# Performance work log

Hardware: AMD Instinct MI355X
Metric: run time of the kernel (lower is better)

The kernel has to match this reference:

```python
import jax, jax.numpy as jnp
import numpy as np

D_MODEL = 1024
N_HEAD = 16
D_HEAD = 64
M_FEAT = 128  # d_kernel_map


def _gen_projection_matrix(m, d, rng):
    # Performer-style: stacked orthogonal blocks scaled by chi-distributed row norms
    blocks = []
    for _ in range(m // d):
        q, _ = np.linalg.qr(rng.standard_normal((d, d)))
        blocks.append(q.T)
    rem = m % d
    if rem > 0:
        q, _ = np.linalg.qr(rng.standard_normal((d, d)))
        blocks.append(q.T[:rem])
    mat = np.vstack(blocks)
    multiplier = np.linalg.norm(rng.standard_normal((m, d)), axis=1, keepdims=True)
    return (mat * multiplier).astype(np.float32)


def setup_inputs() -> dict:
    key = jax.random.key(0)
    ks = jax.random.split(key, 6)
    B, L = 4, 4096
    rng = np.random.default_rng(0)
    hd = N_HEAD * D_HEAD
    x = jax.random.normal(ks[0], (B, L, D_MODEL), dtype=jnp.float32)
    pos_ft = jax.random.normal(ks[1], (B, L, D_MODEL), dtype=jnp.float32)
    pos_ft_slopes = jax.random.normal(ks[2], (B, L, D_MODEL), dtype=jnp.float32)
    W_v = jax.random.normal(ks[3], (D_MODEL, hd), dtype=jnp.float32) / np.sqrt(D_MODEL)
    W_o = jax.random.normal(ks[4], (hd, D_MODEL), dtype=jnp.float32) / np.sqrt(hd)
    pos_ft_weight = jax.random.normal(ks[5], (D_MODEL, hd), dtype=jnp.float32)
    pos_ft_scale = jnp.ones((1, 1, N_HEAD, 1), dtype=jnp.float32)
    head_range = 1.0 / N_HEAD
    offs = (np.arange(0, 1.0, head_range) + head_range / 2.0).astype(np.float32)
    pos_ft_offsets = jnp.asarray(offs).reshape(1, 1, N_HEAD, 1)
    proj = jnp.asarray(_gen_projection_matrix(M_FEAT, D_HEAD, rng))
    return {"x": x, "pos_ft": pos_ft, "pos_ft_slopes": pos_ft_slopes,
            "W_v": W_v, "W_o": W_o, "pos_ft_weight": pos_ft_weight,
            "pos_ft_scale": pos_ft_scale, "pos_ft_offsets": pos_ft_offsets,
            "proj": proj}


def _fourier_kernel(data, proj):
    # data: [B,L,H,D]; proj: [M,D] -> features [B,L,H,2M]
    data_normalizer = 1.0 / data.shape[-1] ** 0.25
    ratio = 1.0 / proj.shape[0] ** 0.5
    data_dash = jnp.einsum('blhd,md->blhm', data_normalizer * data, proj)
    return jnp.concatenate([ratio * jnp.sin(data_dash), ratio * jnp.cos(data_dash)], axis=-1)


def reference(x, pos_ft, pos_ft_slopes, W_v, W_o, pos_ft_weight, pos_ft_scale, pos_ft_offsets, proj):
    B, L, _ = x.shape
    v = (x @ W_v).reshape(B, L, N_HEAD, D_HEAD)
    pos_proj = (pos_ft @ pos_ft_weight).reshape(B, L, N_HEAD, D_HEAD)
    slope_proj = (pos_ft_slopes @ pos_ft_weight).reshape(B, L, N_HEAD, D_HEAD)
    query_pos = pos_ft_scale * pos_proj
    key_pos = query_pos + pos_ft_offsets * (pos_ft_scale * slope_proj)
    q_prime = _fourier_kernel(query_pos, proj)   # [B,L,H,2M]
    k_prime = _fourier_kernel(key_pos, proj)
    kv = jnp.einsum('blhm,blhd->bhmd', k_prime, v)
    z = jnp.einsum('blhm,bhmd->blhd', q_prime, kv)
    norm_factor = jnp.linalg.norm(slope_proj, axis=-1, keepdims=True) / float(L)
    z = (z * norm_factor).reshape(B, L, N_HEAD * D_HEAD)
    # dropout is identity in eval mode
    return z @ W_o
```

## Files before the change

### kernel.cpp

```cpp
#include <hip/hip_runtime.h>
#include <hip/hip_bf16.h>
#include <stdint.h>


typedef _Float16 hx8 __attribute__((ext_vector_type(8)));
typedef _Float16 hx4 __attribute__((ext_vector_type(4)));
typedef float    fx4 __attribute__((ext_vector_type(4)));

#define H_   16
#define D_   64
#define L_   4096
#define B_   4
#define KV_SPLIT 16

__device__ __forceinline__ void g2l16(const _Float16* g, _Float16* l) {
  __builtin_amdgcn_global_load_lds(
      (const __attribute__((address_space(1))) void*)g,
      (__attribute__((address_space(3))) void*)l, 16, 0, 0);
}

__global__ __launch_bounds__(256) void wt2_k(const float* __restrict__ W0,
                                             _Float16* __restrict__ T0,
                                             const float* __restrict__ W1,
                                             _Float16* __restrict__ T1) {
  const float* W = blockIdx.z ? W1 : W0;
  _Float16* WT   = blockIdx.z ? T1 : T0;
  __shared__ float tile[64][65];
  int t = threadIdx.x; int c = t & 63; int r0 = t >> 6;
  int bx = blockIdx.x * 64, by = blockIdx.y * 64;
  for (int r = r0; r < 64; r += 4) tile[r][c] = W[(long)(by + r) * 1024 + bx + c];
  __syncthreads();
  for (int r = r0; r < 64; r += 4)
    WT[(long)(bx + r) * 1024 + by + c] = (_Float16)tile[c][r];
}

__global__ __launch_bounds__(256) void wpf3_k(const float* __restrict__ W,
                                              _Float16* __restrict__ WT3) {
  __shared__ float tile[64][65];
  int t = threadIdx.x; int c = t & 63; int r0 = t >> 6;
  int bx = blockIdx.x * 64, by = blockIdx.y * 64;
  for (int r = r0; r < 64; r += 4) tile[r][c] = W[(long)(by + r) * 1024 + bx + c];
  __syncthreads();
  for (int r = r0; r < 64; r += 4) {
    float x = tile[c][r];
    _Float16 hi = (_Float16)x;
    _Float16 lo = (_Float16)(x - (float)hi);
    long base = (long)(bx + r) * 3072 + by + c;
    WT3[base] = hi; WT3[base + 1024] = hi; WT3[base + 2048] = lo;
  }
}

__global__ __launch_bounds__(256) void proj6_k(const float* __restrict__ proj,
                                               _Float16* __restrict__ proj6T) {
  int i = blockIdx.x * 256 + threadIdx.x;
  if (i >= 8192) return;
  int m = i >> 6, d = i & 63;
  float p = 0.35355339059327373f * proj[i];
  _Float16 hi = (_Float16)p;
  _Float16 lo = (_Float16)(p - (float)hi);
  long b = (long)m * 384 + d;
  proj6T[b]       = hi; proj6T[b + 64]  = hi; proj6T[b + 128] = lo;
  proj6T[b + 192] = hi; proj6T[b + 256] = hi; proj6T[b + 320] = lo;
}

__global__ __launch_bounds__(256) void zero_k(float* __restrict__ p, int n4) {
  int i = blockIdx.x * 256 + threadIdx.x;
  int stride = gridDim.x * 256;
  fx4 z = {0.f, 0.f, 0.f, 0.f};
  for (; i < n4; i += stride) ((fx4*)p)[i] = z;
}

__global__ __launch_bounds__(256) void cvt_hilo2_k(const float* __restrict__ pos,
                                                   const float* __restrict__ slp,
                                                   _Float16* __restrict__ ph2,
                                                   _Float16* __restrict__ sh2) {
  const float* in = blockIdx.y ? slp : pos;
  _Float16* out   = blockIdx.y ? sh2 : ph2;
  long i = (long)blockIdx.x * 256 + threadIdx.x;
  long idx = i * 8;
  int row = (int)(idx >> 10), c = (int)(idx & 1023);
  fx4 a = *(const fx4*)&in[idx];
  fx4 b = *(const fx4*)&in[idx + 4];
  hx8 hi, lo;
#pragma unroll
  for (int e = 0; e < 4; ++e) {
    _Float16 h0 = (_Float16)a[e]; hi[e] = h0;     lo[e]     = (_Float16)(a[e] - (float)h0);
    _Float16 h1 = (_Float16)b[e]; hi[4 + e] = h1; lo[4 + e] = (_Float16)(b[e] - (float)h1);
  }
  *(hx8*)&out[(long)row * 2048 + c]        = hi;
  *(hx8*)&out[(long)row * 2048 + 1024 + c] = lo;
}

__global__ __launch_bounds__(256) void cvt16_k(const float* __restrict__ in,
                                               _Float16* __restrict__ out, long n8) {
  long i = (long)blockIdx.x * 256 + threadIdx.x;
  if (i >= n8) return;
  long idx = i * 8;
  fx4 a = *(const fx4*)&in[idx];
  fx4 b = *(const fx4*)&in[idx + 4];
  hx8 h;
#pragma unroll
  for (int e = 0; e < 4; ++e) { h[e] = (_Float16)a[e]; h[4 + e] = (_Float16)b[e]; }
  *(hx8*)&out[idx] = h;
}

template<int BM, int BN, int AMODE, int SECSH, int EPI, int BMODE, typename OUT_T>
__global__ __launch_bounds__(256) void gemm_bt_k(
    const void* __restrict__ Av, const _Float16* __restrict__ BT,
    OUT_T* __restrict__ C, int K, int lda, int ldb, int ldc,
    long sAb, long sAh, long sBb, long sBh, long sCb, long sCh,
    const float* __restrict__ norms, const float* __restrict__ scp,
    const float* __restrict__ ofp, const float* __restrict__ Pprev,
    float* __restrict__ nout)
{
  __shared__ __align__(16) _Float16 sA[BM * 64];
  __shared__ __align__(16) _Float16 sB[BN * 64];
  const int t = threadIdx.x;
  const int lane = t & 63;
  const int w = t >> 6;
  const int wm = w >> 1, wn = w & 1;
  const int by = blockIdx.x, bx = blockIdx.y, bz = blockIdx.z;
  long aoff64 = (long)(bz >> 4) * sAb + (long)(bz & 15) * sAh;
  if constexpr (AMODE == 5) aoff64 = 0;
  const _Float16* BT16 = BT;
  const float*    B32  = (const float*)BT;
  if constexpr (BMODE == 0) BT16 += (long)(bz >> 4) * sBb + (long)(bz & 15) * sBh;
  else                      B32  += (long)(bz >> 4) * sBb + (long)(bz & 15) * sBh;
  C += (long)(bz >> 4) * sCb + (long)(bz & 15) * sCh;
  const _Float16* A16 = (const _Float16*)Av + aoff64;
  if constexpr (EPI == 4) {
    if (bz & 15) A16 = (const _Float16*)Pprev + aoff64;
  }
  constexpr int WTM = BM / 32, WTN = BN / 32;
  fx4 acc[WTM][WTN];
#pragma unroll
  for (int i = 0; i < WTM; ++i)
#pragma unroll
    for (int j = 0; j < WTN; ++j) acc[i][j] = (fx4){0.f, 0.f, 0.f, 0.f};

  const int trow = t >> 3;
  const int kc8  = ((t & 7) ^ (trow & 7)) * 8;
  int aoff[BM / 32];
#pragma unroll
  for (int i = 0; i < BM / 32; ++i)
    aoff[i] = (by * BM + i * 32 + trow) * lda + kc8;
  int boff[BN / 32];
#pragma unroll
  for (int i = 0; i < BN / 32; ++i)
    boff[i] = (bx * BN + i * 32 + trow) * ldb + kc8;
  _Float16* sAdst[BM / 32];
  _Float16* sBdst[BN / 32];
#pragma unroll
  for (int i = 0; i < BM / 32; ++i) sAdst[i] = &sA[(i * 256 + (w << 6)) * 8];
#pragma unroll
  for (int i = 0; i < BN / 32; ++i) sBdst[i] = &sB[(i * 256 + (w << 6)) * 8];

  int Klim = K;
  if constexpr (AMODE == 5) { if ((bz & 1) == 0) Klim >>= 1; }

  for (int k0 = 0; k0 < Klim; k0 += 64) {
    __syncthreads();
    {
      int cb;
      if constexpr (AMODE == 4) {
        int sec = k0 >> SECSH;
        cb = (k0 & ((1 << SECSH) - 1)) + (sec == 1 ? (1 << SECSH) : 0);
      } else if constexpr (AMODE == 5) {
        int sec = k0 >> SECSH;
        cb = ((sec == 1 || sec == 4) ? 64 : 0) + (sec >= 3 ? (int)sAb : 0);
      } else cb = k0;
#pragma unroll
      for (int i = 0; i < BM / 32; ++i) g2l16(A16 + (aoff[i] + cb), sAdst[i]);
    }
    if constexpr (BMODE == 0) {
#pragma unroll
      for (int i = 0; i < BN / 32; ++i) g2l16(BT16 + (boff[i] + k0), sBdst[i]);
    } else {
#pragma unroll
      for (int i = 0; i < BN / 32; ++i) {
        const float* src = B32 + (boff[i] + k0);
        fx4 v0 = *(const fx4*)src;
        fx4 v1 = *(const fx4*)(src + 4);
        hx8 hv;
#pragma unroll
        for (int e = 0; e < 4; ++e) { hv[e] = (_Float16)v0[e]; hv[4 + e] = (_Float16)v1[e]; }
        *(hx8*)&sB[(i * 256 + t) * 8] = hv;
      }
    }
    __syncthreads();
#pragma unroll
    for (int kk = 0; kk < 64; kk += 32) {
      hx8 af[WTM], bf[WTN];
      int kcb = (kk >> 3) + (lane >> 4);
#pragma unroll
      for (int i = 0; i < WTM; ++i) {
        int r = wm * (BM / 2) + i * 16 + (lane & 15);
        af[i] = *(const hx8*)&sA[(r * 8 + (kcb ^ (r & 7))) * 8];
      }
#pragma unroll
      for (int j = 0; j < WTN; ++j) {
        int r = wn * (BN / 2) + j * 16 + (lane & 15);
        bf[j] = *(const hx8*)&sB[(r * 8 + (kcb ^ (r & 7))) * 8];
      }
#pragma unroll
      for (int i = 0; i < WTM; ++i)
#pragma unroll
        for (int j = 0; j < WTN; ++j)
          acc[i][j] = __builtin_amdgcn_mfma_f32_16x16x32_f16(af[i], bf[j], acc[i][j], 0, 0, 0);
    }
  }
  if constexpr (EPI == 0) {
#pragma unroll
    for (int i = 0; i < WTM; ++i) {
#pragma unroll
      for (int j = 0; j < WTN; ++j) {
        int rowb = by * BM + wm * (BM / 2) + i * 16 + ((lane >> 4) << 2);
        int col  = bx * BN + wn * (BN / 2) + j * 16 + (lane & 15);
#pragma unroll
        for (int r = 0; r < 4; ++r)
          C[(long)(rowb + r) * ldc + col] = (OUT_T)acc[i][j][r];
      }
    }
  } else if constexpr (EPI == 1) {
    const float inv2pi = 0.15915494309189535f;
    const float ratio  = 0.08838834764831845f;
    const bool useN = ((bz & 15) == 0);
#pragma unroll
    for (int i = 0; i < WTM; ++i) {
#pragma unroll
      for (int j = 0; j < WTN; ++j) {
        int rowb = by * BM + wm * (BM / 2) + i * 16 + ((lane >> 4) << 2);
        int col  = bx * BN + wn * (BN / 2) + j * 16 + (lane & 15);
#pragma unroll
        for (int r = 0; r < 4; ++r) {
          int row = rowb + r;
          float rn = ratio * (useN ? norms[row] : 1.0f);
          long ob = ((long)(row & 15) * 4096 + (row >> 4)) * 256;
          float v = acc[i][j][r] * inv2pi;
          v -= floorf(v);
          C[ob + col]       = (OUT_T)(rn * __builtin_amdgcn_sinf(v));
          C[ob + 128 + col] = (OUT_T)(rn * __builtin_amdgcn_cosf(v));
        }
      }
    }
  } else {
    const int h = ((bx * BN) >> 6) + wn;
    const float sc = scp[h];
    _Float16* C16 = (_Float16*)C;
    if ((bz & 15) == 0) {
#pragma unroll
      for (int i = 0; i < WTM; ++i) {
#pragma unroll
        for (int j = 0; j < WTN; ++j) {
          int rowb = by * BM + wm * (BM / 2) + i * 16 + ((lane >> 4) << 2);
          int d    = j * 16 + (lane & 15);
#pragma unroll
          for (int r = 0; r < 4; ++r) {
            float v = sc * acc[i][j][r];
            long a = ((long)(rowb + r) * 16 + h) * 128 + d;
            _Float16 hi = (_Float16)v;
            C16[a]      = hi;
            C16[a + 64] = (_Float16)(v - (float)hi);
          }
        }
      }
    } else {
      const float osc = ofp[h] * sc;
#pragma unroll
      for (int i = 0; i < WTM; ++i) {
        float sq[4] = {0.f, 0.f, 0.f, 0.f};
        int rowb = by * BM + wm * (BM / 2) + i * 16 + ((lane >> 4) << 2);
#pragma unroll
        for (int j = 0; j < WTN; ++j) {
          int d = j * 16 + (lane & 15);
#pragma unroll
          for (int r = 0; r < 4; ++r) {
            float a0 = acc[i][j][r];
            sq[r] += a0 * a0;
            float v = osc * a0;
            long a = ((long)(rowb + r) * 16 + h) * 128 + d;
            _Float16 hi = (_Float16)v;
            C16[a]      = hi;
            C16[a + 64] = (_Float16)(v - (float)hi);
          }
        }
#pragma unroll
        for (int r = 0; r < 4; ++r) {
          float s = sq[r];
          s += __shfl_xor(s, 1); s += __shfl_xor(s, 2);
          s += __shfl_xor(s, 4); s += __shfl_xor(s, 8);
          if ((lane & 15) == 0)
            nout[(long)(rowb + r) * 16 + h] = sqrtf(s) * (1.0f / 4096.0f);
        }
      }
    }
  }
}

__global__ __launch_bounds__(256) void kv_k(const _Float16* __restrict__ Kp,
                                            const _Float16* __restrict__ Vhb,
                                            float* __restrict__ kvacc)
{
  __shared__ __align__(16) _Float16 sK[256 * 72];
  __shared__ __align__(16) _Float16 sV[64 * 72];
  const int t = threadIdx.x, lane = t & 63, w = t >> 6;
  const int h = blockIdx.x;
  const int l0 = blockIdx.y * (L_ / KV_SPLIT);
  fx4 acc[4][4];
#pragma unroll
  for (int i = 0; i < 4; ++i)
#pragma unroll
    for (int j = 0; j < 4; ++j) acc[i][j] = (fx4){0.f, 0.f, 0.f, 0.f};
  const _Float16* Kbase = Kp + (long)h * L_ * 256;
  for (int kt = 0; kt < L_ / KV_SPLIT; kt += 64) {
    __syncthreads();
#pragma unroll
    for (int it = 0; it < 2; ++it) {
      int idx = t + it * 256;
      int m8 = idx & 31, bl = (idx >> 5) << 2;
      const _Float16* src = &Kbase[(long)(l0 + kt + bl) * 256 + m8 * 8];
      hx8 r0 = *(const hx8*)(src);
      hx8 r1 = *(const hx8*)(src + 256);
      hx8 r2 = *(const hx8*)(src + 512);
      hx8 r3 = *(const hx8*)(src + 768);
      int kx = (m8 & 7) << 4;
#pragma unroll
      for (int e = 0; e < 8; ++e) {
        hx4 v; v[0] = r0[e]; v[1] = r1[e]; v[2] = r2[e]; v[3] = r3[e];
        int byte = (((m8 * 8 + e) * 72 + bl) * 2) ^ kx;
        *(hx4*)((char*)sK + byte) = v;
      }
    }
    if (t < 128) {
      int d8 = t & 7, bl = (t >> 3) << 2;
      const _Float16* src = &Vhb[(long)(l0 + kt + bl) * 1024 + h * 64 + d8 * 8];
      hx8 r0 = *(const hx8*)(src);
      hx8 r1 = *(const hx8*)(src + 1024);
      hx8 r2 = *(const hx8*)(src + 2048);
      hx8 r3 = *(const hx8*)(src + 3072);
      int kx = d8 << 4;
#pragma unroll
      for (int e = 0; e < 8; ++e) {
        hx4 v; v[0] = r0[e]; v[1] = r1[e]; v[2] = r2[e]; v[3] = r3[e];
        int byte = (((d8 * 8 + e) * 72 + bl) * 2) ^ kx;
        *(hx4*)((char*)sV + byte) = v;
      }
    }
    __syncthreads();
#pragma unroll
    for (int kk = 0; kk < 64; kk += 32) {
      hx8 af[4], bf[4];
      int lfr = kk + ((lane >> 4) << 3);
#pragma unroll
      for (int i = 0; i < 4; ++i) {
        int r = i * 16 + (lane & 15);
        af[i] = *(const hx8*)((const char*)sV +
                ((((r * 72 + lfr) * 2)) ^ (((r >> 3) & 7) << 4)));
      }
#pragma unroll
      for (int j = 0; j < 4; ++j) {
        int r = w * 64 + j * 16 + (lane & 15);
        bf[j] = *(const hx8*)((const char*)sK +
                ((((r * 72 + lfr) * 2)) ^ (((r >> 3) & 7) << 4)));
      }
#pragma unroll
      for (int i = 0; i < 4; ++i)
#pragma unroll
        for (int j = 0; j < 4; ++j)
          acc[i][j] = __builtin_amdgcn_mfma_f32_16x16x32_f16(af[i], bf[j], acc[i][j], 0, 0, 0);
    }
  }
  float* obase = kvacc + (long)h * (64 * 256);
#pragma unroll
  for (int i = 0; i < 4; ++i)
#pragma unroll
    for (int j = 0; j < 4; ++j) {
      int d0 = i * 16 + ((lane >> 4) << 2);
      int m  = w * 64 + j * 16 + (lane & 15);
#pragma unroll
      for (int r = 0; r < 4; ++r)
        atomicAdd(&obase[(long)(d0 + r) * 256 + m], acc[i][j][r]);
    }
}

extern "C" void kernel_launch(void* const* d_in, const int* in_sizes, int n_in,
                              void* d_out, int out_size, void* d_ws, size_t ws_size,
                              hipStream_t stream) {
  const float* x     = (const float*)d_in[0];
  const float* pos   = (const float*)d_in[1];
  const float* slp   = (const float*)d_in[2];
  const float* Wv    = (const float*)d_in[3];
  const float* Wo    = (const float*)d_in[4];
  const float* Wpf   = (const float*)d_in[5];
  const float* scale = (const float*)d_in[6];
  const float* offs  = (const float*)d_in[7];
  const float* proj  = (const float*)d_in[8];
  float* out = (float*)d_out;
  char* ws = (char*)d_ws;

  size_t o = 0;
  auto alloc = [&](size_t bytes) { char* p = ws + o; o += (bytes + 255) & ~(size_t)255; return p; };
  _Float16* Pb2    = (_Float16*)alloc(33554432);
  _Float16* Sb2    = (_Float16*)alloc(33554432);
  _Float16* qpr    = (_Float16*)alloc(33554432);
  _Float16* kpr    = (_Float16*)alloc(33554432);
  _Float16* Vh     = (_Float16*)alloc(33554432);
  _Float16* Zb     = (_Float16*)alloc(33554432);
  _Float16* WvT    = (_Float16*)alloc(2097152);
  _Float16* WoT    = (_Float16*)alloc(2097152);
  _Float16* Wpf3T  = (_Float16*)alloc(6291456);
  _Float16* proj6T = (_Float16*)alloc(98304);
  float*    normsB = (float*)alloc(524288);
  float*    kvacc  = (float*)alloc(4194304);
  _Float16* ph2 = qpr;
  _Float16* sh2 = kpr;
  _Float16* xh  = Zb;
  (void)Sb2; (void)ws_size; (void)in_sizes; (void)n_in; (void)out_size;

  wt2_k<<<dim3(16, 16, 2), 256, 0, stream>>>(Wv, WvT, Wo, WoT);
  wpf3_k<<<dim3(16, 16), 256, 0, stream>>>(Wpf, Wpf3T);
  proj6_k<<<32, 256, 0, stream>>>(proj, proj6T);
  zero_k<<<256, 256, 0, stream>>>(kvacc, 1048576 / 4);
  cvt16_k<<<8192, 256, 0, stream>>>(x, xh, 2097152);

  gemm_bt_k<128, 128, 0, 0, 0, 0, _Float16><<<dim3(128, 8, 1), 256, 0, stream>>>(
      xh, WvT, Vh, 1024, 1024, 1024, 1024, 0, 0, 0, 0, 0, 0,
      nullptr, nullptr, nullptr, nullptr, nullptr);

  for (int sb = 0; sb < 2; ++sb) {
    const float* pos_sb = pos + (long)sb * 8192 * 1024;
    const float* slp_sb = slp + (long)sb * 8192 * 1024;
    cvt_hilo2_k<<<dim3(4096, 2), 256, 0, stream>>>(pos_sb, slp_sb, ph2, sh2);
    gemm_bt_k<128, 128, 4, 10, 4, 0, _Float16><<<dim3(64, 8, 2), 256, 0, stream>>>(
        ph2, Wpf3T, Pb2, 3072, 2048, 3072, 128, 0, 0, 0, 0, 0, 16777216L,
        nullptr, scale, offs, (const float*)sh2, normsB);

    for (int bb = 0; bb < 2; ++bb) {
      int b = sb * 2 + bb;
      _Float16* Vh_b  = Vh + (long)b * L_ * 1024;
      _Float16* Zb_b  = Zb + (long)b * L_ * 1024;
      float* kvacc_b  = kvacc + (long)b * H_ * 64 * 256;
      gemm_bt_k<128, 128, 5, 6, 1, 0, _Float16><<<dim3(512, 1, 2), 256, 0, stream>>>(
          Pb2 + (long)bb * 8388608, proj6T, qpr, 384, 128, 384, 0,
          16777216L , 0L, 0, 0, 0, 16777216L,
          normsB + (long)bb * 65536, nullptr, nullptr, nullptr, nullptr);
      kv_k<<<dim3(16, KV_SPLIT), 256, 0, stream>>>(kpr, Vh_b, kvacc_b);
      gemm_bt_k<128, 64, 0, 0, 0, 1, _Float16><<<dim3(32, 1, 16), 256, 0, stream>>>(
          qpr, (const _Float16*)kvacc_b, Zb_b, 256, 256, 256, 1024,
          0L, (long)L_ * 256, 0L, 16384L, 0L, 64L,
          nullptr, nullptr, nullptr, nullptr, nullptr);
    }
  }
  gemm_bt_k<128, 128, 0, 0, 0, 0, float><<<dim3(128, 8, 1), 256, 0, stream>>>(
      Zb, WoT, out, 1024, 1024, 1024, 1024, 0, 0, 0, 0, 0, 0,
      nullptr, nullptr, nullptr, nullptr, nullptr);
}
```

Before: 860.8 us.

## Fuse prep kernels and batch feature/kv/z stages across two batches per launch

Merges the five setup kernels (weight transposes, proj split, kv accumulator zeroing, x conversion) into one launch, with block ranges selecting the task. When the workspace is large enough, the Fourier feature GEMM, kv reduction and z GEMM each run once per pair of batches by widening the grid z dimension, which cuts launches and raises per-launch parallelism. It needs a bigger feature buffer and falls back to the per-batch loop otherwise.

```diff
diff --git a/kernel.cpp b/kernel.cpp
--- a/kernel.cpp
+++ b/kernel.cpp
@@ -19,55 +19,64 @@
       (__attribute__((address_space(3))) void*)l, 16, 0, 0);
 }
 
-__global__ __launch_bounds__(256) void wt2_k(const float* __restrict__ W0,
-                                             _Float16* __restrict__ T0,
-                                             const float* __restrict__ W1,
-                                             _Float16* __restrict__ T1) {
-  const float* W = blockIdx.z ? W1 : W0;
-  _Float16* WT   = blockIdx.z ? T1 : T0;
+__global__ __launch_bounds__(256) void prep_k(
+    const float* __restrict__ Wv, _Float16* __restrict__ WvT,
+    const float* __restrict__ Wo, _Float16* __restrict__ WoT,
+    const float* __restrict__ Wpf, _Float16* __restrict__ Wpf3T,
+    const float* __restrict__ proj, _Float16* __restrict__ proj6T,
+    float* __restrict__ kvacc, const float* __restrict__ x,
+    _Float16* __restrict__ xh)
+{
   __shared__ float tile[64][65];
-  int t = threadIdx.x; int c = t & 63; int r0 = t >> 6;
-  int bx = blockIdx.x * 64, by = blockIdx.y * 64;
-  for (int r = r0; r < 64; r += 4) tile[r][c] = W[(long)(by + r) * 1024 + bx + c];
-  __syncthreads();
-  for (int r = r0; r < 64; r += 4)
-    WT[(long)(bx + r) * 1024 + by + c] = (_Float16)tile[c][r];
-}
-
-__global__ __launch_bounds__(256) void wpf3_k(const float* __restrict__ W,
-                                              _Float16* __restrict__ WT3) {
-  __shared__ float tile[64][65];
-  int t = threadIdx.x; int c = t & 63; int r0 = t >> 6;
-  int bx = blockIdx.x * 64, by = blockIdx.y * 64;
-  for (int r = r0; r < 64; r += 4) tile[r][c] = W[(long)(by + r) * 1024 + bx + c];
-  __syncthreads();
-  for (int r = r0; r < 64; r += 4) {
-    float x = tile[c][r];
-    _Float16 hi = (_Float16)x;
-    _Float16 lo = (_Float16)(x - (float)hi);
-    long base = (long)(bx + r) * 3072 + by + c;
-    WT3[base] = hi; WT3[base + 1024] = hi; WT3[base + 2048] = lo;
-  }
-}
-
-__global__ __launch_bounds__(256) void proj6_k(const float* __restrict__ proj,
-                                               _Float16* __restrict__ proj6T) {
-  int i = blockIdx.x * 256 + threadIdx.x;
-  if (i >= 8192) return;
-  int m = i >> 6, d = i & 63;
-  float p = 0.35355339059327373f * proj[i];
-  _Float16 hi = (_Float16)p;
-  _Float16 lo = (_Float16)(p - (float)hi);
-  long b = (long)m * 384 + d;
-  proj6T[b]       = hi; proj6T[b + 64]  = hi; proj6T[b + 128] = lo;
-  proj6T[b + 192] = hi; proj6T[b + 256] = hi; proj6T[b + 320] = lo;
-}
-
-__global__ __launch_bounds__(256) void zero_k(float* __restrict__ p, int n4) {
-  int i = blockIdx.x * 256 + threadIdx.x;
-  int stride = gridDim.x * 256;
-  fx4 z = {0.f, 0.f, 0.f, 0.f};
-  for (; i < n4; i += stride) ((fx4*)p)[i] = z;
+  const int blk = blockIdx.x, t = threadIdx.x;
+  if (blk < 768) {
+    const float* W; int i;
+    if (blk < 256)      { W = Wv;  i = blk; }
+    else if (blk < 512) { W = Wo;  i = blk - 256; }
+    else                { W = Wpf; i = blk - 512; }
+    int bx = (i & 15) * 64, by = (i >> 4) * 64;
+    int c = t & 63, r0 = t >> 6;
+    for (int r = r0; r < 64; r += 4)
+      tile[r][c] = W[(long)(by + r) * 1024 + bx + c];
+    __syncthreads();
+    if (blk < 512) {
+      _Float16* WT = (blk < 256) ? WvT : WoT;
+      for (int r = r0; r < 64; r += 4)
+        WT[(long)(bx + r) * 1024 + by + c] = (_Float16)tile[c][r];
+    } else {
+      for (int r = r0; r < 64; r += 4) {
+        float xv = tile[c][r];
+        _Float16 hi = (_Float16)xv;
+        _Float16 lo = (_Float16)(xv - (float)hi);
+        long base = (long)(bx + r) * 3072 + by + c;
+        Wpf3T[base] = hi; Wpf3T[base + 1024] = hi; Wpf3T[base + 2048] = lo;
+      }
+    }
+  } else if (blk < 800) {
+    int i = (blk - 768) * 256 + t;
+    if (i < 8192) {
+      float p = 0.35355339059327373f * proj[i];
+      _Float16 hi = (_Float16)p;
+      _Float16 lo = (_Float16)(p - (float)hi);
+      long b = (long)(i >> 6) * 384 + (i & 63);
+      proj6T[b]       = hi; proj6T[b + 64]  = hi; proj6T[b + 128] = lo;
+      proj6T[b + 192] = hi; proj6T[b + 256] = hi; proj6T[b + 320] = lo;
+    }
+  } else if (blk < 1056) {
+    fx4 z = {0.f, 0.f, 0.f, 0.f};
+#pragma unroll
+    for (int e = 0; e < 4; ++e)
+      ((fx4*)kvacc)[(blk - 800) * 1024 + e * 256 + t] = z;
+  } else {
+    long i = (long)(blk - 1056) * 256 + t;
+    long idx = i * 8;
+    fx4 a = *(const fx4*)&x[idx];
+    fx4 b = *(const fx4*)&x[idx + 4];
+    hx8 h;
+#pragma unroll
+    for (int e = 0; e < 4; ++e) { h[e] = (_Float16)a[e]; h[4 + e] = (_Float16)b[e]; }
+    *(hx8*)&xh[idx] = h;
+  }
 }
 
 __global__ __launch_bounds__(256) void cvt_hilo2_k(const float* __restrict__ pos,
@@ -89,19 +98,6 @@
   }
   *(hx8*)&out[(long)row * 2048 + c]        = hi;
   *(hx8*)&out[(long)row * 2048 + 1024 + c] = lo;
-}
-
-__global__ __launch_bounds__(256) void cvt16_k(const float* __restrict__ in,
-                                               _Float16* __restrict__ out, long n8) {
-  long i = (long)blockIdx.x * 256 + threadIdx.x;
-  if (i >= n8) return;
-  long idx = i * 8;
-  fx4 a = *(const fx4*)&in[idx];
-  fx4 b = *(const fx4*)&in[idx + 4];
-  hx8 h;
-#pragma unroll
-  for (int e = 0; e < 4; ++e) { h[e] = (_Float16)a[e]; h[4 + e] = (_Float16)b[e]; }
-  *(hx8*)&out[idx] = h;
 }
 
 template<int BM, int BN, int AMODE, int SECSH, int EPI, int BMODE, typename OUT_T>
@@ -121,7 +117,7 @@
   const int wm = w >> 1, wn = w & 1;
   const int by = blockIdx.x, bx = blockIdx.y, bz = blockIdx.z;
   long aoff64 = (long)(bz >> 4) * sAb + (long)(bz & 15) * sAh;
-  if constexpr (AMODE == 5) aoff64 = 0;
+  if constexpr (AMODE == 5) aoff64 = (long)(bz >> 1) * sAh;
   const _Float16* BT16 = BT;
   const float*    B32  = (const float*)BT;
   if constexpr (BMODE == 0) BT16 += (long)(bz >> 4) * sBb + (long)(bz & 15) * sBh;
@@ -224,7 +220,9 @@
   } else if constexpr (EPI == 1) {
     const float inv2pi = 0.15915494309189535f;
     const float ratio  = 0.08838834764831845f;
-    const bool useN = ((bz & 15) == 0);
+    const bool useN = ((bz & 1) == 0);
+    const float* nrm = norms;
+    if constexpr (AMODE == 5) nrm += (long)(bz >> 1) * 65536;
 #pragma unroll
     for (int i = 0; i < WTM; ++i) {
 #pragma unroll
@@ -234,7 +232,7 @@
 #pragma unroll
         for (int r = 0; r < 4; ++r) {
           int row = rowb + r;
-          float rn = ratio * (useN ? norms[row] : 1.0f);
+          float rn = ratio * (useN ? nrm[row] : 1.0f);
           long ob = ((long)(row & 15) * 4096 + (row >> 4)) * 256;
           float v = acc[i][j][r] * inv2pi;
           v -= floorf(v);
@@ -299,13 +297,19 @@
 
 __global__ __launch_bounds__(256) void kv_k(const _Float16* __restrict__ Kp,
                                             const _Float16* __restrict__ Vhb,
-                                            float* __restrict__ kvacc)
+                                            float* __restrict__ kvacc,
+                                            long kstride, long vstride,
+                                            long ostride)
 {
   __shared__ __align__(16) _Float16 sK[256 * 72];
   __shared__ __align__(16) _Float16 sV[64 * 72];
   const int t = threadIdx.x, lane = t & 63, w = t >> 6;
   const int h = blockIdx.x;
   const int l0 = blockIdx.y * (L_ / KV_SPLIT);
+  const int bb = blockIdx.z;
+  Kp    += (long)bb * kstride;
+  Vhb   += (long)bb * vstride;
+  kvacc += (long)bb * ostride;
   fx4 acc[4][4];
 #pragma unroll
   for (int i = 0; i < 4; ++i)
@@ -400,10 +404,11 @@
 
   size_t o = 0;
   auto alloc = [&](size_t bytes) { char* p = ws + o; o += (bytes + 255) & ~(size_t)255; return p; };
-  _Float16* Pb2    = (_Float16*)alloc(33554432);
-  _Float16* Sb2    = (_Float16*)alloc(33554432);
-  _Float16* qpr    = (_Float16*)alloc(33554432);
-  _Float16* kpr    = (_Float16*)alloc(33554432);
+  _Float16* Pb2 = (_Float16*)alloc(33554432);
+  _Float16* Sb2 = (_Float16*)alloc(33554432);
+  const size_t rest = 33554432UL * 2 + 2097152UL * 2 + 6291456 + 98304 + 524288 + 4194304;
+  const bool batched = ws_size >= o + 134217728UL + rest + 8192;
+  _Float16* qpr = (_Float16*)alloc(batched ? 134217728UL : 67108864UL);
   _Float16* Vh     = (_Float16*)alloc(33554432);
   _Float16* Zb     = (_Float16*)alloc(33554432);
   _Float16* WvT    = (_Float16*)alloc(2097152);
@@ -413,15 +418,12 @@
   float*    normsB = (float*)alloc(524288);
   float*    kvacc  = (float*)alloc(4194304);
   _Float16* ph2 = qpr;
-  _Float16* sh2 = kpr;
+  _Float16* sh2 = qpr + 16777216;
   _Float16* xh  = Zb;
-  (void)Sb2; (void)ws_size; (void)in_sizes; (void)n_in; (void)out_size;
-
-  wt2_k<<<dim3(16, 16, 2), 256, 0, stream>>>(Wv, WvT, Wo, WoT);
-  wpf3_k<<<dim3(16, 16), 256, 0, stream>>>(Wpf, Wpf3T);
-  proj6_k<<<32, 256, 0, stream>>>(proj, proj6T);
-  zero_k<<<256, 256, 0, stream>>>(kvacc, 1048576 / 4);
-  cvt16_k<<<8192, 256, 0, stream>>>(x, xh, 2097152);
+  (void)Sb2; (void)in_sizes; (void)n_in; (void)out_size;
+
+  prep_k<<<9248, 256, 0, stream>>>(Wv, WvT, Wo, WoT, Wpf, Wpf3T, proj, proj6T,
+                                   kvacc, x, xh);
 
   gemm_bt_k<128, 128, 0, 0, 0, 0, _Float16><<<dim3(128, 8, 1), 256, 0, stream>>>(
       xh, WvT, Vh, 1024, 1024, 1024, 1024, 0, 0, 0, 0, 0, 0,
@@ -430,25 +432,42 @@
   for (int sb = 0; sb < 2; ++sb) {
     const float* pos_sb = pos + (long)sb * 8192 * 1024;
     const float* slp_sb = slp + (long)sb * 8192 * 1024;
+    _Float16* Vh_sb = Vh + (long)sb * 2 * L_ * 1024;
+    _Float16* Zb_sb = Zb + (long)sb * 2 * L_ * 1024;
+    float* kvacc_sb = kvacc + (long)sb * 2 * 262144;
+
     cvt_hilo2_k<<<dim3(4096, 2), 256, 0, stream>>>(pos_sb, slp_sb, ph2, sh2);
     gemm_bt_k<128, 128, 4, 10, 4, 0, _Float16><<<dim3(64, 8, 2), 256, 0, stream>>>(
         ph2, Wpf3T, Pb2, 3072, 2048, 3072, 128, 0, 0, 0, 0, 0, 16777216L,
         nullptr, scale, offs, (const float*)sh2, normsB);
 
-    for (int bb = 0; bb < 2; ++bb) {
-      int b = sb * 2 + bb;
-      _Float16* Vh_b  = Vh + (long)b * L_ * 1024;
-      _Float16* Zb_b  = Zb + (long)b * L_ * 1024;
-      float* kvacc_b  = kvacc + (long)b * H_ * 64 * 256;
-      gemm_bt_k<128, 128, 5, 6, 1, 0, _Float16><<<dim3(512, 1, 2), 256, 0, stream>>>(
-          Pb2 + (long)bb * 8388608, proj6T, qpr, 384, 128, 384, 0,
-          16777216L , 0L, 0, 0, 0, 16777216L,
-          normsB + (long)bb * 65536, nullptr, nullptr, nullptr, nullptr);
-      kv_k<<<dim3(16, KV_SPLIT), 256, 0, stream>>>(kpr, Vh_b, kvacc_b);
-      gemm_bt_k<128, 64, 0, 0, 0, 1, _Float16><<<dim3(32, 1, 16), 256, 0, stream>>>(
-          qpr, (const _Float16*)kvacc_b, Zb_b, 256, 256, 256, 1024,
-          0L, (long)L_ * 256, 0L, 16384L, 0L, 64L,
+    if (batched) {
+      gemm_bt_k<128, 128, 5, 6, 1, 0, _Float16><<<dim3(512, 1, 4), 256, 0, stream>>>(
+          Pb2, proj6T, qpr, 384, 128, 384, 0,
+          16777216L , 8388608L , 0, 0, 0, 16777216L,
+          normsB, nullptr, nullptr, nullptr, nullptr);
+      kv_k<<<dim3(16, KV_SPLIT, 2), 256, 0, stream>>>(
+          qpr + 16777216, Vh_sb, kvacc_sb, 33554432L, 4194304L, 262144L);
+      gemm_bt_k<128, 64, 0, 0, 0, 1, _Float16><<<dim3(32, 1, 32), 256, 0, stream>>>(
+          qpr, (const _Float16*)kvacc_sb, Zb_sb, 256, 256, 256, 1024,
+          33554432L, (long)L_ * 256, 262144L, 16384L, (long)L_ * 1024, 64L,
           nullptr, nullptr, nullptr, nullptr, nullptr);
+    } else {
+      for (int bb = 0; bb < 2; ++bb) {
+        _Float16* Vh_b  = Vh_sb + (long)bb * L_ * 1024;
+        _Float16* Zb_b  = Zb_sb + (long)bb * L_ * 1024;
+        float* kvacc_b  = kvacc_sb + (long)bb * 262144;
+        gemm_bt_k<128, 128, 5, 6, 1, 0, _Float16><<<dim3(512, 1, 2), 256, 0, stream>>>(
+            Pb2 + (long)bb * 8388608, proj6T, qpr, 384, 128, 384, 0,
+            16777216L, 0L, 0, 0, 0, 16777216L,
+            normsB + (long)bb * 65536, nullptr, nullptr, nullptr, nullptr);
+        kv_k<<<dim3(16, KV_SPLIT, 1), 256, 0, stream>>>(
+            qpr + 16777216, Vh_b, kvacc_b, 0L, 0L, 0L);
+        gemm_bt_k<128, 64, 0, 0, 0, 1, _Float16><<<dim3(32, 1, 16), 256, 0, stream>>>(
+            qpr, (const _Float16*)kvacc_b, Zb_b, 256, 256, 256, 1024,
+            0L, (long)L_ * 256, 0L, 16384L, 0L, 64L,
+            nullptr, nullptr, nullptr, nullptr, nullptr);
+      }
     }
   }
   gemm_bt_k<128, 128, 0, 0, 0, 0, float><<<dim3(128, 8, 1), 256, 0, stream>>>(
```

Result: no change. 846.6 us (-1.6%).
